# Performance work log

Hardware: AMD Instinct MI355X
Metric: run time of the kernel (lower is better)

The kernel has to match this reference:

```python
import jax, jax.numpy as jnp
import numpy as np

B, S, HID = 2, 2048, 4096
NH, NKV = 32, 8
HD = HID // NH          # 128
GROUPS = NH // NKV      # 4


def rotate_half(x):
    x1, x2 = x[..., : x.shape[-1] // 2], x[..., x.shape[-1] // 2 :]
    return jnp.concatenate((-x2, x1), axis=-1)


def apply_rope(x, cos, sin):
    # x: (B,H,S,D); cos/sin: (B,S,D) -> (B,1,S,D)
    c = cos[:, None, :, :]
    s = sin[:, None, :, :]
    return x * c + rotate_half(x) * s


def setup_inputs() -> dict:
    key = jax.random.key(0)
    ks = jax.random.split(key, 12)
    scale = 1.0 / np.sqrt(HID)
    return {
        "hidden_states": jax.random.normal(ks[0], (B, S, HID), jnp.float32),
        "cos": jax.random.uniform(ks[1], (B, S, HD), jnp.float32),
        "sin": jax.random.uniform(ks[2], (B, S, HD), jnp.float32),
        "Wq": jax.random.normal(ks[3], (HID, NH * HD), jnp.float32) * scale,
        "bq": jax.random.normal(ks[4], (NH * HD,), jnp.float32) * 0.01,
        "Wk": jax.random.normal(ks[5], (HID, NKV * HD), jnp.float32) * scale,
        "bk": jax.random.normal(ks[6], (NKV * HD,), jnp.float32) * 0.01,
        "Wv": jax.random.normal(ks[7], (HID, NKV * HD), jnp.float32) * scale,
        "bv": jax.random.normal(ks[8], (NKV * HD,), jnp.float32) * 0.01,
        "Wo": jax.random.normal(ks[9], (NH * HD, HID), jnp.float32) * scale,
    }


def reference(hidden_states, cos, sin, Wq, bq, Wk, bk, Wv, bv, Wo):
    b, s, _ = hidden_states.shape
    q = (hidden_states @ Wq + bq).reshape(b, s, NH, HD).transpose(0, 2, 1, 3)
    k = (hidden_states @ Wk + bk).reshape(b, s, NKV, HD).transpose(0, 2, 1, 3)
    v = (hidden_states @ Wv + bv).reshape(b, s, NKV, HD).transpose(0, 2, 1, 3)
    q = apply_rope(q, cos, sin)
    k = apply_rope(k, cos, sin)
    # GQA: repeat_interleave along head dim
    k = jnp.repeat(k, GROUPS, axis=1)
    v = jnp.repeat(v, GROUPS, axis=1)
    scores = jnp.einsum("bhqd,bhkd->bhqk", q, k) / np.sqrt(HD).astype(np.float32)
    weights = jax.nn.softmax(scores, axis=-1)  # NOTE: no causal mask, per source
    out = jnp.einsum("bhqk,bhkd->bhqd", weights, v)
    out = out.transpose(0, 2, 1, 3).reshape(b, s, NH * HD)
    return out @ Wo
```

## Files before the change

### kernel.cpp

```cpp
#include <hip/hip_runtime.h>
#include <stdint.h>

#define Bz   2
#define Ss   2048
#define HID  4096
#define NH   32
#define NKV  8
#define HD   128
#define Mrows (Bz*Ss)
#define NQKV 6144

typedef __attribute__((ext_vector_type(8))) short b16x8;
typedef __attribute__((ext_vector_type(8))) _Float16 f16x8;
typedef __attribute__((ext_vector_type(4))) float f32x4;

__device__ __forceinline__ unsigned short f2bf(float f) {
  union { float f; uint32_t u; } v; v.f = f;
  uint32_t r = v.u + 0x7FFFu + ((v.u >> 16) & 1u);
  return (unsigned short)(r >> 16);
}

__device__ __forceinline__ void cp16(const void* g, void* l) {
  __builtin_amdgcn_global_load_lds(
      (const __attribute__((address_space(1))) void*)g,
      (__attribute__((address_space(3))) void*)l, 16, 0, 0);
}

__global__ __launch_bounds__(256) void cast_x(const float* __restrict__ x,
                                              unsigned short* __restrict__ o) {
  int i = blockIdx.x*256 + threadIdx.x;
  float4 v = ((const float4*)x)[i];
  ushort4 r; r.x = f2bf(v.x); r.y = f2bf(v.y); r.z = f2bf(v.z); r.w = f2bf(v.w);
  ((ushort4*)o)[i] = r;
}

__global__ __launch_bounds__(256) void wtrans(const float* __restrict__ W,
                                              unsigned short* __restrict__ Wt,
                                              int K, int N) {
  __shared__ float t[32][33];
  int n0 = blockIdx.x*32, k0 = blockIdx.y*32;
  int tx = threadIdx.x & 31, ty = threadIdx.x >> 5;
#pragma unroll
  for (int i = 0; i < 4; i++)
    t[ty + i*8][tx] = W[(size_t)(k0 + ty + i*8)*N + n0 + tx];
  __syncthreads();
#pragma unroll
  for (int i = 0; i < 4; i++)
    Wt[(size_t)(n0 + ty + i*8)*K + k0 + tx] = f2bf(t[tx][ty + i*8]);
}

__global__ __launch_bounds__(256) void bias_cat(const float* __restrict__ bq,
                                                const float* __restrict__ bk,
                                                const float* __restrict__ bv,
                                                float* __restrict__ o) {
  int i = blockIdx.x*256 + threadIdx.x;
  float v = (i < 4096) ? bq[i] : (i < 5120) ? bk[i-4096] : bv[i-5120];
  o[i] = v;
}

__global__ __launch_bounds__(512, 2) void gemm_bt(const unsigned short* __restrict__ A,
                                                  const unsigned short* __restrict__ Bt,
                                                  const float* __restrict__ bias,
                                                  float* __restrict__ C,
                                                  int N, int K) {
  __shared__ __align__(16) short Al[2*16384];
  __shared__ __align__(16) short Bl[2*16384];
  const int tid = threadIdx.x;
  const int w = tid >> 6, lane = tid & 63;
  const int wm = w >> 2, wn = w & 3;
  const int lrow = lane & 15, quad = lane >> 4;
  const int swz = lrow & 7;
  int bid = blockIdx.y * gridDim.x + blockIdx.x;
  const int nwg = gridDim.x * gridDim.y;
  bid = (bid & 7) * (nwg >> 3) + (bid >> 3);
  const int m0 = (bid / gridDim.x) * 256;
  const int n0 = (bid % gridDim.x) * 256;
  const int srA = (tid >> 3) & 63;
  const int srB = (tid >> 3) & 31;
  const int gcA = (tid & 7) ^ (srA & 7);
  const int gcB = (tid & 7) ^ (srB & 7);
  const unsigned short* gaA = A  + (size_t)(m0 + srA)*K + gcA*8;
  const unsigned short* gaB = Bt + (size_t)(n0 + (tid >> 8)*64 + srB)*K + gcB*8;
  const int wbs = w*512;

#define SB0() __builtin_amdgcn_sched_barrier(0)
#define STAGE_A(buf, t, h) do {                                                         \
    cp16(gaA + (size_t)((h)*64      )*K + (size_t)(t)*64, Al + (buf)*16384 + (h)*8192        + wbs); \
    cp16(gaA + (size_t)((h)*64 + 128)*K + (size_t)(t)*64, Al + (buf)*16384 + (h)*8192 + 4096 + wbs); \
  } while (0)
#define STAGE_B(buf, t, h) do {                                                         \
    cp16(gaB + (size_t)((h)*32      )*K + (size_t)(t)*64, Bl + (buf)*16384 + (h)*8192        + wbs); \
    cp16(gaB + (size_t)((h)*32 + 128)*K + (size_t)(t)*64, Bl + (buf)*16384 + (h)*8192 + 4096 + wbs); \
  } while (0)

  const short* Ar = Al + wm*4096 + lrow*64;
  const short* Br = Bl + wn*2048 + lrow*64;
  const int kc0 = (quad ^ swz) * 8;
  const int NT = K >> 6;
  f32x4 acc[8][4] = {};

  STAGE_A(0, 0, 0); SB0(); STAGE_B(0, 0, 0); SB0();
  STAGE_B(0, 0, 1); SB0(); STAGE_A(0, 0, 1); SB0();
  if (NT > 1) { STAGE_A(1, 1, 0); SB0(); STAGE_B(1, 1, 0); SB0(); STAGE_B(1, 1, 1); SB0(); }
  if (NT > 1) { asm volatile("s_waitcnt vmcnt(6)" ::: "memory"); }
  else        { asm volatile("s_waitcnt vmcnt(0)" ::: "memory"); }
  __builtin_amdgcn_s_barrier();
  SB0();

  for (int t = 0; t < NT; ++t) {
    const int cb = (t & 1) * 16384;
    b16x8 a0[4][2], a1[4][2], b0[2][2], b1[2][2];
#pragma unroll
    for (int mi = 0; mi < 4; mi++) {
      a0[mi][0] = *(const b16x8*)(Ar + cb + mi*1024 + kc0);
      a0[mi][1] = *(const b16x8*)(Ar + cb + mi*1024 + (kc0 ^ 32));
    }
#pragma unroll
    for (int ni = 0; ni < 2; ni++) {
      b0[ni][0] = *(const b16x8*)(Br + cb + ni*1024 + kc0);
      b0[ni][1] = *(const b16x8*)(Br + cb + ni*1024 + (kc0 ^ 32));
    }
    if (t + 1 < NT) STAGE_A((t + 1) & 1, t + 1, 1);
    __builtin_amdgcn_s_barrier();
    asm volatile("s_waitcnt lgkmcnt(0)" ::: "memory");
    SB0();
    __builtin_amdgcn_s_setprio(1);
#pragma unroll
    for (int mi = 0; mi < 4; mi++)
#pragma unroll
      for (int ni = 0; ni < 2; ni++) {
        acc[mi][ni] = __builtin_amdgcn_mfma_f32_16x16x32_bf16(a0[mi][0], b0[ni][0], acc[mi][ni], 0, 0, 0);
        acc[mi][ni] = __builtin_amdgcn_mfma_f32_16x16x32_bf16(a0[mi][1], b0[ni][1], acc[mi][ni], 0, 0, 0);
      }
    __builtin_amdgcn_s_setprio(0);
    __builtin_amdgcn_s_barrier();
#pragma unroll
    for (int ni = 0; ni < 2; ni++) {
      b1[ni][0] = *(const b16x8*)(Br + cb + 8192 + ni*1024 + kc0);
      b1[ni][1] = *(const b16x8*)(Br + cb + 8192 + ni*1024 + (kc0 ^ 32));
    }
    if (t + 2 < NT) STAGE_A(t & 1, t + 2, 0);
    __builtin_amdgcn_s_barrier();
    asm volatile("s_waitcnt lgkmcnt(0)" ::: "memory");
    SB0();
    __builtin_amdgcn_s_setprio(1);
#pragma unroll
    for (int mi = 0; mi < 4; mi++)
#pragma unroll
      for (int ni = 0; ni < 2; ni++) {
        acc[mi][ni+2] = __builtin_amdgcn_mfma_f32_16x16x32_bf16(a0[mi][0], b1[ni][0], acc[mi][ni+2], 0, 0, 0);
        acc[mi][ni+2] = __builtin_amdgcn_mfma_f32_16x16x32_bf16(a0[mi][1], b1[ni][1], acc[mi][ni+2], 0, 0, 0);
      }
    __builtin_amdgcn_s_setprio(0);
    __builtin_amdgcn_s_barrier();
#pragma unroll
    for (int mi = 0; mi < 4; mi++) {
      a1[mi][0] = *(const b16x8*)(Ar + cb + 8192 + mi*1024 + kc0);
      a1[mi][1] = *(const b16x8*)(Ar + cb + 8192 + mi*1024 + (kc0 ^ 32));
    }
    if (t + 2 < NT) STAGE_B(t & 1, t + 2, 0);
    __builtin_amdgcn_s_barrier();
    asm volatile("s_waitcnt lgkmcnt(0)" ::: "memory");
    SB0();
    __builtin_amdgcn_s_setprio(1);
#pragma unroll
    for (int mi = 0; mi < 4; mi++)
#pragma unroll
      for (int ni = 0; ni < 2; ni++) {
        acc[mi+4][ni] = __builtin_amdgcn_mfma_f32_16x16x32_bf16(a1[mi][0], b0[ni][0], acc[mi+4][ni], 0, 0, 0);
        acc[mi+4][ni] = __builtin_amdgcn_mfma_f32_16x16x32_bf16(a1[mi][1], b0[ni][1], acc[mi+4][ni], 0, 0, 0);
      }
    __builtin_amdgcn_s_setprio(0);
    __builtin_amdgcn_s_barrier();
    if (t + 2 < NT) {
      STAGE_B(t & 1, t + 2, 1);
      asm volatile("s_waitcnt vmcnt(6)" ::: "memory");
    } else {
      asm volatile("s_waitcnt vmcnt(0)" ::: "memory");
    }
    __builtin_amdgcn_s_barrier();
    SB0();
    __builtin_amdgcn_s_setprio(1);
#pragma unroll
    for (int mi = 0; mi < 4; mi++)
#pragma unroll
      for (int ni = 0; ni < 2; ni++) {
        acc[mi+4][ni+2] = __builtin_amdgcn_mfma_f32_16x16x32_bf16(a1[mi][0], b1[ni][0], acc[mi+4][ni+2], 0, 0, 0);
        acc[mi+4][ni+2] = __builtin_amdgcn_mfma_f32_16x16x32_bf16(a1[mi][1], b1[ni][1], acc[mi+4][ni+2], 0, 0, 0);
      }
    __builtin_amdgcn_s_setprio(0);
    __builtin_amdgcn_s_barrier();
    SB0();
  }
#undef STAGE_A
#undef STAGE_B
#undef SB0

#pragma unroll
  for (int mi = 0; mi < 8; mi++)
#pragma unroll
    for (int ni = 0; ni < 4; ni++) {
      int col = n0 + wn*64 + ni*16 + lrow;
      float bv = bias ? bias[col] : 0.0f;
#pragma unroll
      for (int r = 0; r < 4; r++) {
        int row = m0 + wm*128 + mi*16 + quad*4 + r;
        C[(size_t)row*N + col] = acc[mi][ni][r] + bv;
      }
    }
}

__global__ __launch_bounds__(256) void rope(const float* __restrict__ X, int xstride, int colbase,
                                            const float* __restrict__ cp,
                                            const float* __restrict__ sp,
                                            unsigned short* __restrict__ o, int nh, float scale) {
  int tid = blockIdx.x*256 + threadIdx.x;
  int d = tid & 63;
  int h = (tid >> 6) % nh;
  int m = tid / (64*nh);
  int b = m >> 11, s = m & 2047;
  size_t xoff = (size_t)m*xstride + colbase + (size_t)h*HD + d;
  float x1 = X[xoff], x2 = X[xoff + 64];
  const float* cb = cp + ((size_t)b*Ss + s)*HD;
  const float* sb = sp + ((size_t)b*Ss + s)*HD;
  float o1 = (x1*cb[d]      - x2*sb[d])      * scale;
  float o2 = (x2*cb[d + 64] + x1*sb[d + 64]) * scale;
  unsigned short* ob = o + ((size_t)(b*nh + h)*Ss + s)*HD;
  ob[d]      = f2bf(o1);
  ob[d + 64] = f2bf(o2);
}

__global__ __launch_bounds__(256) void vprep(const float* __restrict__ Vf, int xstride, int colbase,
                                             _Float16* __restrict__ Vt) {
  __shared__ float t[32][33];
  int dt = blockIdx.x, st = blockIdx.y, bk = blockIdx.z;
  int b = bk >> 3, kvh = bk & 7;
  int tx = threadIdx.x & 31, ty = threadIdx.x >> 5;
#pragma unroll
  for (int i = 0; i < 4; i++) {
    int s = st*32 + ty + i*8;
    t[ty + i*8][tx] = Vf[(size_t)(b*Ss + s)*xstride + colbase + kvh*HD + dt*32 + tx];
  }
  __syncthreads();
#pragma unroll
  for (int i = 0; i < 4; i++) {
    int d = dt*32 + ty + i*8;
    Vt[((size_t)bk*HD + d)*Ss + st*32 + tx] = (_Float16)t[tx][ty + i*8];
  }
}

__global__ __launch_bounds__(256) void flash(const unsigned short* __restrict__ Qr,
                                             const unsigned short* __restrict__ Kr,
                                             const _Float16* __restrict__ Vt,
                                             unsigned short* __restrict__ AO) {
  __shared__ short Kl[64*128];
  __shared__ short Vl[144*64];
  __shared__ _Float16 Pl[4][16*72];
  const int qt = blockIdx.x, h = blockIdx.y, b = blockIdx.z;
  const int tid = threadIdx.x, w = tid >> 6, lane = tid & 63;
  const int lrow = lane & 15, quad = lane >> 4;
  const int wb = tid & 192;
  const int swz = lrow & 7;
  const int kvh = h >> 2;
  const unsigned short* Qb = Qr + ((size_t)(b*NH + h)*Ss + qt*64 + w*16)*HD;
  const unsigned short* Kb = Kr + ((size_t)(b*NKV + kvh)*Ss)*HD;
  const _Float16*       Vb = Vt + ((size_t)(b*NKV + kvh)*HD)*Ss;
  {
    int idx = tid*4;
    int row = 128 + (idx >> 6);
    unsigned short v = (row == 128) ? 0x3C00u : 0u;
    ushort4 vv; vv.x = v; vv.y = v; vv.z = v; vv.w = v;
    *(ushort4*)((unsigned short*)Vl + 128*64 + idx) = vv;
  }
  b16x8 qf[4];
#pragma unroll
  for (int t = 0; t < 4; t++)
    qf[t] = *(const b16x8*)(Qb + (size_t)lrow*HD + t*32 + quad*8);
  f32x4 o[8] = {};
  f32x4 ol = {};
  for (int kt = 0; kt < 32; kt++) {
    __syncthreads();
#pragma unroll
    for (int i = 0; i < 4; i++) {
      int c = i*256 + tid;
      int r = c >> 4, gc = (c & 15) ^ (r & 7);
      cp16(Kb + (size_t)(kt*64 + r)*HD + gc*8, Kl + (i*256 + wb)*8);
    }
#pragma unroll
    for (int i = 0; i < 4; i++) {
      int c = i*256 + tid;
      int r = c >> 3, gc = (c & 7) ^ (r & 7);
      cp16(Vb + (size_t)r*Ss + kt*64 + gc*8, Vl + (i*256 + wb)*8);
    }
    __syncthreads();
    f32x4 sc[4] = {};
#pragma unroll
    for (int t = 0; t < 4; t++)
#pragma unroll
      for (int n = 0; n < 4; n++) {
        b16x8 kf = *(const b16x8*)(Kl + (n*16 + lrow)*128 + ((t*4 + quad) ^ swz)*8);
        sc[n] = __builtin_amdgcn_mfma_f32_16x16x32_bf16(qf[t], kf, sc[n], 0, 0, 0);
      }
#pragma unroll
    for (int n = 0; n < 4; n++)
#pragma unroll
      for (int r = 0; r < 4; r++)
        Pl[w][(quad*4 + r)*72 + n*16 + lrow] = (_Float16)__builtin_amdgcn_exp2f(sc[n][r]);
#pragma unroll
    for (int st = 0; st < 2; st++) {
      f16x8 pf = *(const f16x8*)(&Pl[w][lrow*72 + st*32 + quad*8]);
#pragma unroll
      for (int n = 0; n < 8; n++) {
        f16x8 vf = *(const f16x8*)((const _Float16*)Vl + (n*16 + lrow)*64 + ((st*4 + quad) ^ swz)*8);
        o[n] = __builtin_amdgcn_mfma_f32_16x16x32_f16(pf, vf, o[n], 0, 0, 0);
      }
      f16x8 vf1 = *(const f16x8*)((const _Float16*)Vl + (128 + lrow)*64 + ((st*4 + quad) ^ swz)*8);
      ol = __builtin_amdgcn_mfma_f32_16x16x32_f16(pf, vf1, ol, 0, 0, 0);
    }
  }
  float rl[4];
#pragma unroll
  for (int r = 0; r < 4; r++)
    rl[r] = 1.0f / __shfl(ol[r], lane & 48);
  const int s0 = qt*64 + w*16;
#pragma unroll
  for (int n = 0; n < 8; n++)
#pragma unroll
    for (int r = 0; r < 4; r++) {
      int srow = s0 + quad*4 + r;
      float v = o[n][r] * rl[r];
      AO[((size_t)(b*Ss + srow))*HID + h*HD + n*16 + lrow] = f2bf(v);
    }
}

extern "C" void kernel_launch(void* const* d_in, const int* in_sizes, int n_in,
                              void* d_out, int out_size, void* d_ws, size_t ws_size,
                              hipStream_t stream) {
  (void)in_sizes; (void)n_in; (void)out_size; (void)ws_size;
  const float* hs   = (const float*)d_in[0];
  const float* cosp = (const float*)d_in[1];
  const float* sinp = (const float*)d_in[2];
  const float* Wq   = (const float*)d_in[3];
  const float* bq   = (const float*)d_in[4];
  const float* Wk   = (const float*)d_in[5];
  const float* bk   = (const float*)d_in[6];
  const float* Wv   = (const float*)d_in[7];
  const float* bv   = (const float*)d_in[8];
  const float* Wo   = (const float*)d_in[9];
  float* out = (float*)d_out;
  const float QSC = 0.12751742826919558f;

  char* p = (char*)d_ws;
  unsigned short* Xb   = (unsigned short*)p; p += (size_t)Mrows*HID*2;
  unsigned short* Wcat = (unsigned short*)p; p += (size_t)NQKV*HID*2;
  unsigned short* Wot  = (unsigned short*)p; p += (size_t)HID*HID*2;
  float* bcat = (float*)p; p += (size_t)NQKV*4;
  float* QKVf = (float*)p; p += (size_t)Mrows*NQKV*4;
  unsigned short* Qr = Xb;
  unsigned short* Kr = Wcat;
  _Float16*       Vt = (_Float16*)(Wcat + (size_t)(Bz*NKV)*Ss*HD);
  unsigned short* AO = (unsigned short*)QKVf;

  cast_x<<<Mrows*HID/1024, 256, 0, stream>>>(hs, Xb);
  wtrans<<<dim3(HID/32, HID/32),      256, 0, stream>>>(Wq, Wcat,                        HID, HID);
  wtrans<<<dim3((NKV*HD)/32, HID/32), 256, 0, stream>>>(Wk, Wcat + (size_t)4096*HID,     HID, NKV*HD);
  wtrans<<<dim3((NKV*HD)/32, HID/32), 256, 0, stream>>>(Wv, Wcat + (size_t)5120*HID,     HID, NKV*HD);
  wtrans<<<dim3(HID/32, HID/32),      256, 0, stream>>>(Wo, Wot, HID, HID);
  bias_cat<<<NQKV/256, 256, 0, stream>>>(bq, bk, bv, bcat);

  gemm_bt<<<dim3(NQKV/256, Mrows/256), 512, 0, stream>>>(Xb, Wcat, bcat, QKVf, NQKV, HID);

  rope<<<(Mrows*NH*64)/256,  256, 0, stream>>>(QKVf, NQKV, 0,    cosp, sinp, Qr, NH,  QSC);
  rope<<<(Mrows*NKV*64)/256, 256, 0, stream>>>(QKVf, NQKV, 4096, cosp, sinp, Kr, NKV, 1.0f);
  vprep<<<dim3(HD/32, Ss/32, Bz*NKV), 256, 0, stream>>>(QKVf, NQKV, 5120, Vt);

  flash<<<dim3(Ss/64, NH, Bz), 256, 0, stream>>>(Qr, Kr, Vt, AO);

  gemm_bt<<<dim3(HID/256, Mrows/256), 512, 0, stream>>>(AO, Wot, nullptr, out, HID, HID);
}
```

Before: 840.8 us.

## Restructure GEMM main loop: batch global stages and cut per-iteration barriers

The bf16 GEMM main loop now issues all LDS fragment reads for the current tile up front, using partial lgkmcnt waits so MFMAs start as soon as their operands arrive. After one barrier it issues every global-to-LDS copy for tile t+2 at once, instead of interleaving four separate stage groups between four compute phases. This drops the loop from eight workgroup barriers per iteration to two, and simplifies the vmcnt accounting to a single wait. The risk is burstier memory traffic, less overlap between global loads and compute within an iteration, and more fragment registers held live at once.

```diff
diff --git a/kernel.cpp b/kernel.cpp
--- a/kernel.cpp
+++ b/kernel.cpp
@@ -92,6 +92,8 @@
     cp16(gaB + (size_t)((h)*32      )*K + (size_t)(t)*64, Bl + (buf)*16384 + (h)*8192        + wbs); \
     cp16(gaB + (size_t)((h)*32 + 128)*K + (size_t)(t)*64, Bl + (buf)*16384 + (h)*8192 + 4096 + wbs); \
   } while (0)
+#define STAGE_ALL(buf, t) do { STAGE_A(buf, t, 0); STAGE_A(buf, t, 1); \
+                               STAGE_B(buf, t, 0); STAGE_B(buf, t, 1); } while (0)
 
   const short* Ar = Al + wm*4096 + lrow*64;
   const short* Br = Bl + wn*2048 + lrow*64;
@@ -99,11 +101,10 @@
   const int NT = K >> 6;
   f32x4 acc[8][4] = {};
 
-  STAGE_A(0, 0, 0); SB0(); STAGE_B(0, 0, 0); SB0();
-  STAGE_B(0, 0, 1); SB0(); STAGE_A(0, 0, 1); SB0();
-  if (NT > 1) { STAGE_A(1, 1, 0); SB0(); STAGE_B(1, 1, 0); SB0(); STAGE_B(1, 1, 1); SB0(); }
-  if (NT > 1) { asm volatile("s_waitcnt vmcnt(6)" ::: "memory"); }
-  else        { asm volatile("s_waitcnt vmcnt(0)" ::: "memory"); }
+  STAGE_ALL(0, 0);
+  if (NT > 1) STAGE_ALL(1, 1);
+  asm volatile("s_waitcnt vmcnt(8)" ::: "memory");
+  if (NT == 1) asm volatile("s_waitcnt vmcnt(0)" ::: "memory");
   __builtin_amdgcn_s_barrier();
   SB0();
 
@@ -120,9 +121,13 @@
       b0[ni][0] = *(const b16x8*)(Br + cb + ni*1024 + kc0);
       b0[ni][1] = *(const b16x8*)(Br + cb + ni*1024 + (kc0 ^ 32));
     }
-    if (t + 1 < NT) STAGE_A((t + 1) & 1, t + 1, 1);
-    __builtin_amdgcn_s_barrier();
-    asm volatile("s_waitcnt lgkmcnt(0)" ::: "memory");
+    SB0();
+#pragma unroll
+    for (int ni = 0; ni < 2; ni++) {
+      b1[ni][0] = *(const b16x8*)(Br + cb + 8192 + ni*1024 + kc0);
+      b1[ni][1] = *(const b16x8*)(Br + cb + 8192 + ni*1024 + (kc0 ^ 32));
+    }
+    asm volatile("s_waitcnt lgkmcnt(4)" ::: "memory");
     SB0();
     __builtin_amdgcn_s_setprio(1);
 #pragma unroll
@@ -133,15 +138,12 @@
         acc[mi][ni] = __builtin_amdgcn_mfma_f32_16x16x32_bf16(a0[mi][1], b0[ni][1], acc[mi][ni], 0, 0, 0);
       }
     __builtin_amdgcn_s_setprio(0);
-    __builtin_amdgcn_s_barrier();
-#pragma unroll
-    for (int ni = 0; ni < 2; ni++) {
-      b1[ni][0] = *(const b16x8*)(Br + cb + 8192 + ni*1024 + kc0);
-      b1[ni][1] = *(const b16x8*)(Br + cb + 8192 + ni*1024 + (kc0 ^ 32));
-    }
-    if (t + 2 < NT) STAGE_A(t & 1, t + 2, 0);
-    __builtin_amdgcn_s_barrier();
-    asm volatile("s_waitcnt lgkmcnt(0)" ::: "memory");
+#pragma unroll
+    for (int mi = 0; mi < 4; mi++) {
+      a1[mi][0] = *(const b16x8*)(Ar + cb + 8192 + mi*1024 + kc0);
+      a1[mi][1] = *(const b16x8*)(Ar + cb + 8192 + mi*1024 + (kc0 ^ 32));
+    }
+    asm volatile("s_waitcnt lgkmcnt(8)" ::: "memory");
     SB0();
     __builtin_amdgcn_s_setprio(1);
 #pragma unroll
@@ -152,15 +154,11 @@
         acc[mi][ni+2] = __builtin_amdgcn_mfma_f32_16x16x32_bf16(a0[mi][1], b1[ni][1], acc[mi][ni+2], 0, 0, 0);
       }
     __builtin_amdgcn_s_setprio(0);
+    asm volatile("s_waitcnt lgkmcnt(0)" ::: "memory");
+    SB0();
     __builtin_amdgcn_s_barrier();
-#pragma unroll
-    for (int mi = 0; mi < 4; mi++) {
-      a1[mi][0] = *(const b16x8*)(Ar + cb + 8192 + mi*1024 + kc0);
-      a1[mi][1] = *(const b16x8*)(Ar + cb + 8192 + mi*1024 + (kc0 ^ 32));
-    }
-    if (t + 2 < NT) STAGE_B(t & 1, t + 2, 0);
-    __builtin_amdgcn_s_barrier();
-    asm volatile("s_waitcnt lgkmcnt(0)" ::: "memory");
+    SB0();
+    if (t + 2 < NT) STAGE_ALL(t & 1, t + 2);
     SB0();
     __builtin_amdgcn_s_setprio(1);
 #pragma unroll
@@ -170,17 +168,6 @@
         acc[mi+4][ni] = __builtin_amdgcn_mfma_f32_16x16x32_bf16(a1[mi][0], b0[ni][0], acc[mi+4][ni], 0, 0, 0);
         acc[mi+4][ni] = __builtin_amdgcn_mfma_f32_16x16x32_bf16(a1[mi][1], b0[ni][1], acc[mi+4][ni], 0, 0, 0);
       }
-    __builtin_amdgcn_s_setprio(0);
-    __builtin_amdgcn_s_barrier();
-    if (t + 2 < NT) {
-      STAGE_B(t & 1, t + 2, 1);
-      asm volatile("s_waitcnt vmcnt(6)" ::: "memory");
-    } else {
-      asm volatile("s_waitcnt vmcnt(0)" ::: "memory");
-    }
-    __builtin_amdgcn_s_barrier();
-    SB0();
-    __builtin_amdgcn_s_setprio(1);
 #pragma unroll
     for (int mi = 0; mi < 4; mi++)
 #pragma unroll
@@ -189,11 +176,14 @@
         acc[mi+4][ni+2] = __builtin_amdgcn_mfma_f32_16x16x32_bf16(a1[mi][1], b1[ni][1], acc[mi+4][ni+2], 0, 0, 0);
       }
     __builtin_amdgcn_s_setprio(0);
+    if (t + 2 < NT) { asm volatile("s_waitcnt vmcnt(8)" ::: "memory"); }
+    else            { asm volatile("s_waitcnt vmcnt(0)" ::: "memory"); }
     __builtin_amdgcn_s_barrier();
     SB0();
   }
 #undef STAGE_A
 #undef STAGE_B
+#undef STAGE_ALL
 #undef SB0
 
 #pragma unroll
```

Result: no change. 845.5 us (+0.6%).
